# Kernel tuning notes

Hardware: AMD Instinct MI355X
Metric: run time of the kernel (lower is better)

The kernel has to match this reference:

```python
import jax, jax.numpy as jnp
import numpy as np

BETA = 1.0 / np.sqrt(768.0).astype(np.float32)


def setup_inputs() -> dict:
    key = jax.random.key(0)
    k1, k2, k3 = jax.random.split(key, 3)
    x = jax.random.normal(k1, (32, 512, 768), dtype=jnp.float32)
    # torch nn.Linear(dim, n_prototype).weight has shape [n_prototype, dim]
    w_lookup = jax.random.normal(k2, (4096, 768), dtype=jnp.float32) * 0.02
    # torch nn.Linear(n_prototype, dim).weight has shape [dim, n_prototype]
    w_content = jax.random.normal(k3, (768, 4096), dtype=jnp.float32) * 0.02
    return {"x": x, "w_lookup": w_lookup, "w_content": w_content}


def reference(x, w_lookup, w_content):
    # scores: [b, s, n_prototype] = x @ w_lookup^T, scaled by 1/sqrt(dim)
    scores = jnp.einsum("bsd,pd->bsp", x, w_lookup) * jnp.asarray(BETA, x.dtype)
    lookup = jax.nn.softmax(scores, axis=-1)
    # content: [b, s, dim] = lookup @ w_content^T
    content = jnp.einsum("bsp,dp->bsd", lookup, w_content)
    return content  # dropout is identity in eval / p=0.0
```

## Files before the change

kernel.cpp:

```cpp
#include <hip/hip_runtime.h>
#include <hip/hip_bf16.h>


#define NTOK   16384
#define DIM    768
#define NPROT  4096
#define BETA_F 0.03608439182428583f

typedef __bf16 bf16_t;
typedef __bf16 bf16x8 __attribute__((ext_vector_type(8)));
typedef float  floatx4 __attribute__((ext_vector_type(4)));

__device__ __forceinline__ void async_copy16(const bf16_t* g, void* l) {
  __builtin_amdgcn_global_load_lds(
      (__attribute__((address_space(1))) const void*)g,
      (__attribute__((address_space(3))) void*)l, 16, 0, 0);
}

__global__ __launch_bounds__(256) void cvt_all(
    const float* __restrict__ x, const float* __restrict__ wl,
    const float* __restrict__ wc, bf16_t* __restrict__ xb,
    bf16_t* __restrict__ wlb, bf16_t* __restrict__ wcb,
    int nx8, int nw8, int nc8) {
  int i = blockIdx.x * 256 + threadIdx.x;
  const float* in; bf16_t* out; int k;
  if (i < nx8)            { in = x;  out = xb;  k = i; }
  else if (i < nx8 + nw8) { in = wl; out = wlb; k = i - nx8; }
  else if (i < nx8 + nw8 + nc8) { in = wc; out = wcb; k = i - nx8 - nw8; }
  else return;
  const float4* in4 = (const float4*)in;
  float4 a = in4[2 * k], b = in4[2 * k + 1];
  bf16x8 o;
  o[0] = (bf16_t)a.x; o[1] = (bf16_t)a.y; o[2] = (bf16_t)a.z; o[3] = (bf16_t)a.w;
  o[4] = (bf16_t)b.x; o[5] = (bf16_t)b.y; o[6] = (bf16_t)b.z; o[7] = (bf16_t)b.w;
  ((bf16x8*)out)[k] = o;
}

template <int EPI>
__global__ __launch_bounds__(512, 2)
void gemm256(const bf16_t* __restrict__ A, const bf16_t* __restrict__ B,
             void* __restrict__ Cv, float* __restrict__ rowsum,
             const int K, const int N, const int nN) {
  __shared__ char lds[131072];

  const int tid = threadIdx.x;
  const int l   = tid & 63;
  const int w   = tid >> 6;
  const int wr  = w >> 2;
  const int wc  = w & 3;
  const int lr  = l & 15;
  const int lk  = (l >> 4) << 3;

  const int nwg   = gridDim.x;
  const int chunk = nwg >> 3;
  const int wg    = (blockIdx.x & 7) * chunk + (blockIdx.x >> 3);
  const int m0    = (wg / nN) * 256;
  const int n0    = (wg % nN) * 256;

  int aoff[2][2], boff[2][2];
#pragma unroll
  for (int h = 0; h < 2; ++h)
#pragma unroll
    for (int j = 0; j < 2; ++j) {
      const int s     = j * 8 + w;
      const int mfrag = h * 8 + (s >> 1);
      const int ks    = s & 1;
      aoff[h][j] = (m0 + mfrag * 16 + lr) * K + ks * 32 + lk;
      boff[h][j] = (n0 + mfrag * 16 + lr) * K + ks * 32 + lk;
    }

  auto stageA = [&](int slot, int kt, int h) {
#pragma unroll
    for (int j = 0; j < 2; ++j) {
      const int s  = j * 8 + w;
      const int sf = (h * 8 + (s >> 1)) * 2 + (s & 1);
      async_copy16(A + aoff[h][j] + kt * 64, lds + slot * 65536 + sf * 1024);
    }
  };
  auto stageB = [&](int slot, int kt, int h) {
#pragma unroll
    for (int j = 0; j < 2; ++j) {
      const int s  = j * 8 + w;
      const int sf = (h * 8 + (s >> 1)) * 2 + (s & 1);
      async_copy16(B + boff[h][j] + kt * 64,
                   lds + slot * 65536 + 32768 + sf * 1024);
    }
  };

  bf16x8 af[4][2], bg[4][2];
  auto loadA = [&](int slot, int mh) {
#pragma unroll
    for (int q = 0; q < 4; ++q)
#pragma unroll
      for (int ks = 0; ks < 2; ++ks)
        af[q][ks] = *(const bf16x8*)(lds + slot * 65536 +
                        ((mh * 8 + q * 2 + wr) * 2 + ks) * 1024 + l * 16);
  };
  auto loadB = [&](int slot, int nh, int qb) {
#pragma unroll
    for (int q = 0; q < 2; ++q)
#pragma unroll
      for (int ks = 0; ks < 2; ++ks)
        bg[qb + q][ks] = *(const bf16x8*)(lds + slot * 65536 + 32768 +
                        ((nh * 8 + q * 4 + wc) * 2 + ks) * 1024 + l * 16);
  };

  const floatx4 z = {0.f, 0.f, 0.f, 0.f};
  floatx4 acc[8][4];
#pragma unroll
  for (int mt = 0; mt < 8; ++mt)
#pragma unroll
    for (int nt = 0; nt < 4; ++nt) acc[mt][nt] = z;

  auto mma = [&](int mq, int nq) {
    __builtin_amdgcn_s_setprio(1);
#pragma unroll
    for (int q = 0; q < 4; ++q)
#pragma unroll
      for (int r = 0; r < 2; ++r)
#pragma unroll
        for (int ks = 0; ks < 2; ++ks)
          acc[mq * 4 + q][nq * 2 + r] = __builtin_amdgcn_mfma_f32_16x16x32_bf16(
              af[q][ks], bg[nq * 2 + r][ks], acc[mq * 4 + q][nq * 2 + r], 0, 0, 0);
    __builtin_amdgcn_s_setprio(0);
  };

#define BAR()    __builtin_amdgcn_s_barrier()
#define LGKM0()  asm volatile("s_waitcnt lgkmcnt(0)")
#define LGKM8()  asm volatile("s_waitcnt lgkmcnt(8)")
#define VM(n)    asm volatile("s_waitcnt vmcnt(" #n ")" ::: "memory")

  const int T = K >> 6;

  stageA(0, 0, 0); stageB(0, 0, 0); stageB(0, 0, 1); stageA(0, 0, 1);
  stageA(1, 1, 0); stageB(1, 1, 0); stageB(1, 1, 1);
  VM(6);
  BAR();

#pragma unroll 1
  for (int t = 0; t < T - 2; t += 2) {
    loadA(0, 0); loadB(0, 0, 0);
    stageA(1, t + 1, 1);
    LGKM8();
    BAR(); LGKM0(); mma(0, 0); BAR();
    loadB(0, 1, 2);
    stageA(0, t + 2, 0);
    BAR(); LGKM0(); mma(0, 1); BAR();
    loadA(0, 1);
    stageB(0, t + 2, 0);
    BAR(); LGKM0(); mma(1, 1); BAR();
    stageB(0, t + 2, 1);
    BAR(); mma(1, 0); VM(6); BAR();
    loadA(1, 0); loadB(1, 0, 0);
    stageA(0, t + 2, 1);
    LGKM8();
    BAR(); LGKM0(); mma(0, 0); BAR();
    loadB(1, 1, 2);
    stageA(1, t + 3, 0);
    BAR(); LGKM0(); mma(0, 1); BAR();
    loadA(1, 1);
    stageB(1, t + 3, 0);
    BAR(); LGKM0(); mma(1, 1); BAR();
    stageB(1, t + 3, 1);
    BAR(); mma(1, 0); VM(6); BAR();
  }

  loadA(0, 0); loadB(0, 0, 0);
  stageA(1, T - 1, 1);
  LGKM8();
  BAR(); LGKM0(); mma(0, 0); BAR();
  loadB(0, 1, 2);
  BAR(); LGKM0(); mma(0, 1); BAR();
  loadA(0, 1);
  BAR(); LGKM0(); mma(1, 1); BAR();
  BAR(); mma(1, 0); VM(0); BAR();
  loadA(1, 0); loadB(1, 0, 0);
  BAR(); LGKM0(); mma(0, 0); BAR();
  loadB(1, 1, 2);
  BAR(); LGKM0(); mma(0, 1); BAR();
  loadA(1, 1);
  BAR(); LGKM0(); mma(1, 1); BAR();
  mma(1, 0);

#undef BAR
#undef LGKM0
#undef LGKM8
#undef VM

  const int hi4 = (l >> 4) << 2;
  if (EPI == 0) {
    bf16_t* P = (bf16_t*)Cv;
#pragma unroll
    for (int mt = 0; mt < 8; ++mt) {
      const int row = m0 + (mt * 2 + wr) * 16 + hi4;
      float rs[4] = {0.f, 0.f, 0.f, 0.f};
#pragma unroll
      for (int nt = 0; nt < 4; ++nt) {
        const int col = n0 + (nt * 4 + wc) * 16 + lr;
#pragma unroll
        for (int i = 0; i < 4; ++i) {
          const float e = __expf(acc[mt][nt][i] * BETA_F);
          P[(row + i) * N + col] = (bf16_t)e;
          rs[i] += e;
        }
      }
#pragma unroll
      for (int i = 0; i < 4; ++i) {
        float s = rs[i];
        s += __shfl_xor(s, 1);
        s += __shfl_xor(s, 2);
        s += __shfl_xor(s, 4);
        s += __shfl_xor(s, 8);
        if (lr == 0) atomicAdd(&rowsum[row + i], s);
      }
    }
  } else {
    float* O = (float*)Cv;
#pragma unroll
    for (int mt = 0; mt < 8; ++mt) {
      const int row = m0 + (mt * 2 + wr) * 16 + hi4;
#pragma unroll
      for (int i = 0; i < 4; ++i) {
        const float inv = 1.0f / rowsum[row + i];
#pragma unroll
        for (int nt = 0; nt < 4; ++nt)
          O[(row + i) * N + n0 + (nt * 4 + wc) * 16 + lr] = acc[mt][nt][i] * inv;
      }
    }
  }
}

__global__ __launch_bounds__(256) void hopfield_fallback(
    const float* __restrict__ x, const float* __restrict__ wl,
    const float* __restrict__ wc, float* __restrict__ out) {
  __shared__ float  xs[8 * 768];
  __shared__ bf16_t ps[8 * 4096];
  __shared__ float  rs[8];
  const int tid = threadIdx.x;
  const int r0  = blockIdx.x * 8;
  if (tid < 8) rs[tid] = 0.f;
  for (int i = tid; i < 8 * 768; i += 256)
    xs[i] = x[(r0 + (i / 768)) * 768 + (i % 768)];
  __syncthreads();

  float lsum[8] = {0, 0, 0, 0, 0, 0, 0, 0};
  for (int p = tid; p < 4096; p += 256) {
    float s[8] = {0, 0, 0, 0, 0, 0, 0, 0};
    for (int d = 0; d < 768; ++d) {
      const float wv = wl[p * 768 + d];
#pragma unroll
      for (int r = 0; r < 8; ++r) s[r] += xs[r * 768 + d] * wv;
    }
#pragma unroll
    for (int r = 0; r < 8; ++r) {
      const float e = __expf(s[r] * BETA_F);
      ps[r * 4096 + p] = (bf16_t)e;
      lsum[r] += e;
    }
  }
#pragma unroll
  for (int r = 0; r < 8; ++r) atomicAdd(&rs[r], lsum[r]);
  __syncthreads();

  for (int d = tid; d < 768; d += 256) {
    float o[8] = {0, 0, 0, 0, 0, 0, 0, 0};
    for (int p = 0; p < 4096; ++p) {
      const float wv = wc[d * 4096 + p];
#pragma unroll
      for (int r = 0; r < 8; ++r) o[r] += (float)ps[r * 4096 + p] * wv;
    }
#pragma unroll
    for (int r = 0; r < 8; ++r) out[(r0 + r) * 768 + d] = o[r] / rs[r];
  }
}

extern "C" void kernel_launch(void* const* d_in, const int* in_sizes, int n_in,
                              void* d_out, int out_size, void* d_ws, size_t ws_size,
                              hipStream_t stream) {
  (void)in_sizes; (void)n_in; (void)out_size;
  const float* x  = (const float*)d_in[0];
  const float* wl = (const float*)d_in[1];
  const float* wc = (const float*)d_in[2];
  float* out = (float*)d_out;

  const size_t xb_e = (size_t)NTOK * DIM;
  const size_t wl_e = (size_t)NPROT * DIM;
  const size_t wc_e = (size_t)DIM * NPROT;
  const size_t P_e  = (size_t)NTOK * NPROT;
  const size_t need = (xb_e + wl_e + wc_e + P_e) * 2 + (size_t)NTOK * 4;

  if (ws_size >= need) {
    char* ws = (char*)d_ws;
    bf16_t* xb  = (bf16_t*)ws;  ws += xb_e * 2;
    bf16_t* wlb = (bf16_t*)ws;  ws += wl_e * 2;
    bf16_t* wcb = (bf16_t*)ws;  ws += wc_e * 2;
    bf16_t* P   = (bf16_t*)ws;  ws += P_e * 2;
    float* rowsum = (float*)ws;

    hipMemsetAsync(rowsum, 0, NTOK * sizeof(float), stream);
    const int nx8 = (int)(xb_e / 8), nw8 = (int)(wl_e / 8), nc8 = (int)(wc_e / 8);
    cvt_all<<<(nx8 + nw8 + nc8 + 255) / 256, 256, 0, stream>>>(
        x, wl, wc, xb, wlb, wcb, nx8, nw8, nc8);
    gemm256<0><<<dim3((NTOK / 256) * (NPROT / 256)), 512, 0, stream>>>(
        xb, wlb, (void*)P, rowsum, DIM, NPROT, NPROT / 256);
    gemm256<1><<<dim3((NTOK / 256) * (DIM / 256)), 512, 0, stream>>>(
        P, wcb, (void*)out, rowsum, NPROT, DIM, DIM / 256);
  } else {
    hopfield_fallback<<<NTOK / 8, 256, 0, stream>>>(x, wl, wc, out);
  }
}
```

Before: 429.7 us.

## Use 256x192 tiles for second GEMM to fill all CUs

Adds a dedicated gemm192 kernel for the probability-times-content GEMM. It uses 256x192 output tiles so the grid has 256 workgroups instead of 192, matching the CU count. The LDS staging, fragment loads and MFMA schedule are reworked for three N fragments per wave, and the first GEMM is de-templated. The cost is lower per-tile arithmetic intensity and a more irregular inner schedule.

```diff
diff --git a/kernel.cpp b/kernel.cpp
--- a/kernel.cpp
+++ b/kernel.cpp
@@ -36,10 +36,9 @@
   ((bf16x8*)out)[k] = o;
 }
 
-template <int EPI>
 __global__ __launch_bounds__(512, 2)
 void gemm256(const bf16_t* __restrict__ A, const bf16_t* __restrict__ B,
-             void* __restrict__ Cv, float* __restrict__ rowsum,
+             bf16_t* __restrict__ P, float* __restrict__ rowsum,
              const int K, const int N, const int nN) {
   __shared__ char lds[131072];
 
@@ -182,50 +181,176 @@
   BAR(); LGKM0(); mma(1, 1); BAR();
   mma(1, 0);
 
+  const int hi4 = (l >> 4) << 2;
+#pragma unroll
+  for (int mt = 0; mt < 8; ++mt) {
+    const int row = m0 + (mt * 2 + wr) * 16 + hi4;
+    float rs[4] = {0.f, 0.f, 0.f, 0.f};
+#pragma unroll
+    for (int nt = 0; nt < 4; ++nt) {
+      const int col = n0 + (nt * 4 + wc) * 16 + lr;
+#pragma unroll
+      for (int i = 0; i < 4; ++i) {
+        const float e = __expf(acc[mt][nt][i] * BETA_F);
+        P[(row + i) * N + col] = (bf16_t)e;
+        rs[i] += e;
+      }
+    }
+#pragma unroll
+    for (int i = 0; i < 4; ++i) {
+      float s = rs[i];
+      s += __shfl_xor(s, 1);
+      s += __shfl_xor(s, 2);
+      s += __shfl_xor(s, 4);
+      s += __shfl_xor(s, 8);
+      if (lr == 0) atomicAdd(&rowsum[row + i], s);
+    }
+  }
+}
+
+__global__ __launch_bounds__(512, 2)
+void gemm192(const bf16_t* __restrict__ A, const bf16_t* __restrict__ B,
+             float* __restrict__ O, const float* __restrict__ rowsum,
+             const int K, const int N) {
+  __shared__ char lds[114688];
+
+  const int tid = threadIdx.x;
+  const int l   = tid & 63;
+  const int w   = tid >> 6;
+  const int wr  = w >> 2;
+  const int wc  = w & 3;
+  const int lr  = l & 15;
+  const int lk  = (l >> 4) << 3;
+
+  const int wg = (blockIdx.x & 7) * 32 + (blockIdx.x >> 3);
+  const int m0 = (wg >> 2) * 256;
+  const int n0 = (wg & 3) * 192;
+
+  int aoff[2][2];
+#pragma unroll
+  for (int h = 0; h < 2; ++h)
+#pragma unroll
+    for (int j = 0; j < 2; ++j) {
+      const int s     = j * 8 + w;
+      const int mfrag = h * 8 + (s >> 1);
+      const int ks    = s & 1;
+      aoff[h][j] = (m0 + mfrag * 16 + lr) * K + ks * 32 + lk;
+    }
+  int boff[3];
+#pragma unroll
+  for (int t = 0; t < 3; ++t)
+    boff[t] = (n0 + (t * 4 + (w >> 1)) * 16 + lr) * K + (w & 1) * 32 + lk;
+
+  auto stageA = [&](int slot, int kt, int h) {
+#pragma unroll
+    for (int j = 0; j < 2; ++j) {
+      const int s  = j * 8 + w;
+      const int sf = (h * 8 + (s >> 1)) * 2 + (s & 1);
+      async_copy16(A + aoff[h][j] + kt * 64, lds + slot * 57344 + sf * 1024);
+    }
+  };
+  auto stageBt = [&](int slot, int kt, int t) {
+    async_copy16(B + boff[t] + kt * 64,
+                 lds + slot * 57344 + 32768 + (t * 8 + w) * 1024 + l * 16);
+  };
+
+  bf16x8 af[4][2], bg[3][2];
+  auto loadA = [&](int slot, int mh) {
+#pragma unroll
+    for (int q = 0; q < 4; ++q)
+#pragma unroll
+      for (int ks = 0; ks < 2; ++ks)
+        af[q][ks] = *(const bf16x8*)(lds + slot * 57344 +
+                        ((mh * 8 + q * 2 + wr) * 2 + ks) * 1024 + l * 16);
+  };
+  auto loadBn = [&](int slot, int nlo, int ncnt) {
+    for (int r = 0; r < ncnt; ++r)
+#pragma unroll
+      for (int ks = 0; ks < 2; ++ks)
+        bg[nlo + r][ks] = *(const bf16x8*)(lds + slot * 57344 + 32768 +
+                        (((wc * 3 + nlo + r) * 2 + ks) << 10) + l * 16);
+  };
+
+  const floatx4 z = {0.f, 0.f, 0.f, 0.f};
+  floatx4 acc[8][3];
+#pragma unroll
+  for (int mt = 0; mt < 8; ++mt)
+#pragma unroll
+    for (int nt = 0; nt < 3; ++nt) acc[mt][nt] = z;
+
+  auto mma = [&](int mq, int nlo, int ncnt) {
+    __builtin_amdgcn_s_setprio(1);
+#pragma unroll
+    for (int q = 0; q < 4; ++q)
+      for (int r = 0; r < ncnt; ++r)
+#pragma unroll
+        for (int ks = 0; ks < 2; ++ks)
+          acc[mq * 4 + q][nlo + r] = __builtin_amdgcn_mfma_f32_16x16x32_bf16(
+              af[q][ks], bg[nlo + r][ks], acc[mq * 4 + q][nlo + r], 0, 0, 0);
+    __builtin_amdgcn_s_setprio(0);
+  };
+
+  const int T = K >> 6;
+
+  stageA(0, 0, 0); stageA(0, 0, 1);
+  stageBt(0, 0, 0); stageBt(0, 0, 1); stageBt(0, 0, 2);
+  stageA(1, 1, 0);
+  stageBt(1, 1, 0); stageBt(1, 1, 1); stageBt(1, 1, 2);
+  VM(5);
+  BAR();
+
+#pragma unroll 1
+  for (int t = 0; t < T - 2; t += 2) {
+#pragma unroll
+    for (int u = 0; u < 2; ++u) {
+      const int p = u;
+      loadA(p, 0); loadBn(p, 0, 2);
+      stageA(p ^ 1, t + u + 1, 1);
+      LGKM8();
+      BAR(); LGKM0(); mma(0, 0, 2); BAR();
+      loadBn(p, 2, 1);
+      stageA(p, t + u + 2, 0);
+      BAR(); LGKM0(); mma(0, 2, 1); BAR();
+      loadA(p, 1);
+      stageBt(p, t + u + 2, 0); stageBt(p, t + u + 2, 1);
+      BAR(); LGKM0(); mma(1, 0, 2); BAR();
+      stageBt(p, t + u + 2, 2);
+      BAR(); mma(1, 2, 1); VM(5); BAR();
+    }
+  }
+
+  loadA(0, 0); loadBn(0, 0, 2);
+  stageA(1, T - 1, 1);
+  LGKM8();
+  BAR(); LGKM0(); mma(0, 0, 2); BAR();
+  loadBn(0, 2, 1);
+  BAR(); LGKM0(); mma(0, 2, 1); BAR();
+  loadA(0, 1);
+  BAR(); LGKM0(); mma(1, 0, 2); BAR();
+  BAR(); mma(1, 2, 1); VM(0); BAR();
+  loadA(1, 0); loadBn(1, 0, 2);
+  BAR(); LGKM0(); mma(0, 0, 2); BAR();
+  loadBn(1, 2, 1);
+  BAR(); LGKM0(); mma(0, 2, 1); BAR();
+  loadA(1, 1);
+  BAR(); LGKM0(); mma(1, 0, 2); BAR();
+  mma(1, 2, 1);
+
 #undef BAR
 #undef LGKM0
 #undef LGKM8
 #undef VM
 
   const int hi4 = (l >> 4) << 2;
-  if (EPI == 0) {
-    bf16_t* P = (bf16_t*)Cv;
-#pragma unroll
-    for (int mt = 0; mt < 8; ++mt) {
-      const int row = m0 + (mt * 2 + wr) * 16 + hi4;
-      float rs[4] = {0.f, 0.f, 0.f, 0.f};
-#pragma unroll
-      for (int nt = 0; nt < 4; ++nt) {
-        const int col = n0 + (nt * 4 + wc) * 16 + lr;
-#pragma unroll
-        for (int i = 0; i < 4; ++i) {
-          const float e = __expf(acc[mt][nt][i] * BETA_F);
-          P[(row + i) * N + col] = (bf16_t)e;
-          rs[i] += e;
-        }
-      }
-#pragma unroll
-      for (int i = 0; i < 4; ++i) {
-        float s = rs[i];
-        s += __shfl_xor(s, 1);
-        s += __shfl_xor(s, 2);
-        s += __shfl_xor(s, 4);
-        s += __shfl_xor(s, 8);
-        if (lr == 0) atomicAdd(&rowsum[row + i], s);
-      }
-    }
-  } else {
-    float* O = (float*)Cv;
-#pragma unroll
-    for (int mt = 0; mt < 8; ++mt) {
-      const int row = m0 + (mt * 2 + wr) * 16 + hi4;
-#pragma unroll
-      for (int i = 0; i < 4; ++i) {
-        const float inv = 1.0f / rowsum[row + i];
-#pragma unroll
-        for (int nt = 0; nt < 4; ++nt)
-          O[(row + i) * N + n0 + (nt * 4 + wc) * 16 + lr] = acc[mt][nt][i] * inv;
-      }
+#pragma unroll
+  for (int mt = 0; mt < 8; ++mt) {
+    const int row = m0 + (mt * 2 + wr) * 16 + hi4;
+#pragma unroll
+    for (int i = 0; i < 4; ++i) {
+      const float inv = 1.0f / rowsum[row + i];
+#pragma unroll
+      for (int nt = 0; nt < 3; ++nt)
+        O[(row + i) * N + n0 + (wc * 3 + nt) * 16 + lr] = acc[mt][nt][i] * inv;
     }
   }
 }
@@ -301,10 +426,10 @@
     const int nx8 = (int)(xb_e / 8), nw8 = (int)(wl_e / 8), nc8 = (int)(wc_e / 8);
     cvt_all<<<(nx8 + nw8 + nc8 + 255) / 256, 256, 0, stream>>>(
         x, wl, wc, xb, wlb, wcb, nx8, nw8, nc8);
-    gemm256<0><<<dim3((NTOK / 256) * (NPROT / 256)), 512, 0, stream>>>(
-        xb, wlb, (void*)P, rowsum, DIM, NPROT, NPROT / 256);
-    gemm256<1><<<dim3((NTOK / 256) * (DIM / 256)), 512, 0, stream>>>(
-        P, wcb, (void*)out, rowsum, NPROT, DIM, DIM / 256);
+    gemm256<<<dim3((NTOK / 256) * (NPROT / 256)), 512, 0, stream>>>(
+        xb, wlb, P, rowsum, DIM, NPROT, NPROT / 256);
+    gemm192<<<dim3(256), 512, 0, stream>>>(
+        P, wcb, out, rowsum, NPROT, DIM);
   } else {
     hopfield_fallback<<<NTOK / 8, 256, 0, stream>>>(x, wl, wc, out);
   }
```

Result: faster. 415.0 us (-3.4%).
